# Kernel optimization log

Measured on AMD Instinct MI355X. Metric: run time of the kernel, lower is better.

The kernel has to match this reference:

```python
import jax, jax.numpy as jnp
import numpy as np

B, N, D, M = 16, 4096, 640, 64  # D = hidden_dim*2 + u_in = 2*256 + 128


def setup_inputs() -> dict:
    key = jax.random.key(0)
    kx, kk, kv = jax.random.split(key, 3)
    x = jax.random.normal(kx, (B, N, D), dtype=jnp.float32)
    Mk = jax.random.normal(kk, (M, D), dtype=jnp.float32)
    Mv = jax.random.normal(kv, (M, D), dtype=jnp.float32)
    return {"x": x, "Mk": Mk, "Mv": Mv}


def reference(x, Mk, Mv):
    # scores: [B, N, M] = x @ Mk^T
    scores = jnp.einsum('bnd,md->bnm', x, Mk)
    weights = jax.nn.softmax(scores, axis=-1)
    # out: [B, N, D] = weights @ Mv
    out = jnp.einsum('bnm,md->bnd', weights, Mv)
    return out
```

## Files before the change

kernel.cpp:

```cpp
#include <hip/hip_runtime.h>

typedef float  f32x4  __attribute__((ext_vector_type(4)));
typedef short  short8 __attribute__((ext_vector_type(8)));
typedef __bf16 bf16x8 __attribute__((ext_vector_type(8)));

#define DEV static __device__ __forceinline__

DEV f32x4 mfma16(short8 a, short8 b, f32x4 c) {
  return __builtin_amdgcn_mfma_f32_16x16x32_bf16(
      __builtin_bit_cast(bf16x8, a), __builtin_bit_cast(bf16x8, b), c, 0, 0, 0);
}

DEV void splitf(float f, unsigned short& hi, unsigned short& lo) {
  unsigned u = __builtin_bit_cast(unsigned, f);
  hi = (unsigned short)(u >> 16);
  float hf = __builtin_bit_cast(float, u & 0xFFFF0000u);
  float r = f - hf;
  unsigned v = __builtin_bit_cast(unsigned, r);
  lo = (unsigned short)((v + 0x7FFFu + ((v >> 16) & 1u)) >> 16);
}

#define DDIM 640
#define KCH  20
#define MKP_ELEMS (KCH*2*4*64*8)
#define MVP_OFF   MKP_ELEMS

__global__ void ea_pack(const float* __restrict__ Mk, const float* __restrict__ Mv,
                        unsigned short* __restrict__ ws) {
  int tid = blockIdx.x * 256 + threadIdx.x;
  unsigned short* MkP = ws;
  unsigned short* MvP = ws + MVP_OFF;
  if (tid < 5120) {
    int c = tid >> 8;
    int g = (tid >> 6) & 3;
    int l = tid & 63;
    int t = l & 15, q = l >> 4;
    const float* src = Mk + (16*g + t) * DDIM + 32*c + 8*q;
    unsigned short* dh = MkP + (((c*2 + 0)*4 + g)*64 + l)*8;
    unsigned short* dl = MkP + (((c*2 + 1)*4 + g)*64 + l)*8;
#pragma unroll
    for (int j = 0; j < 8; ++j) splitf(src[j], dh[j], dl[j]);
  } else if (tid < 10240) {
    int s = tid - 5120;
    int n = s >> 7;
    int c = (s >> 6) & 1;
    int l = s & 63;
    int t = l & 15, q = l >> 4;
    const float* src = Mv + (32*c + 8*q) * DDIM + 16*n + t;
    unsigned short* dh = MvP + (((n*2 + c)*2 + 0)*64 + l)*8;
    unsigned short* dl = MvP + (((n*2 + c)*2 + 1)*64 + l)*8;
#pragma unroll
    for (int j = 0; j < 8; ++j) splitf(src[j*DDIM], dh[j], dl[j]);
  }
}

#define LOADX(X0, X1, c) { X0 = *(const f32x4*)(xp + 32*(c)); \
                           X1 = *(const f32x4*)(xp + 32*(c) + 4); }

#define LOADF(c) { const unsigned short* mkc_ = MkP + (c)*4096 + l*8;        \
  fh0 = *(const short8*)(mkc_);        fh1 = *(const short8*)(mkc_ + 512);   \
  fh2 = *(const short8*)(mkc_ + 1024); fh3 = *(const short8*)(mkc_ + 1536);  \
  fl0 = *(const short8*)(mkc_ + 2048); fl1 = *(const short8*)(mkc_ + 2560);  \
  fl2 = *(const short8*)(mkc_ + 3072); fl3 = *(const short8*)(mkc_ + 3584); }

#define SPLITX(X0, X1)                                                       \
  splitf(X0[0], ah.u[0], al.u[0]); splitf(X0[1], ah.u[1], al.u[1]);          \
  splitf(X0[2], ah.u[2], al.u[2]); splitf(X0[3], ah.u[3], al.u[3]);          \
  splitf(X1[0], ah.u[4], al.u[4]); splitf(X1[1], ah.u[5], al.u[5]);          \
  splitf(X1[2], ah.u[6], al.u[6]); splitf(X1[3], ah.u[7], al.u[7]);

#define MFMAS()                                                              \
  acc[0] = mfma16(ah.s, fh0, acc[0]); acc[1] = mfma16(ah.s, fh1, acc[1]);    \
  acc[2] = mfma16(ah.s, fh2, acc[2]); acc[3] = mfma16(ah.s, fh3, acc[3]);    \
  acc[0] = mfma16(al.s, fh0, acc[0]); acc[1] = mfma16(al.s, fh1, acc[1]);    \
  acc[2] = mfma16(al.s, fh2, acc[2]); acc[3] = mfma16(al.s, fh3, acc[3]);    \
  acc[0] = mfma16(ah.s, fl0, acc[0]); acc[1] = mfma16(ah.s, fl1, acc[1]);    \
  acc[2] = mfma16(ah.s, fl2, acc[2]); acc[3] = mfma16(ah.s, fl3, acc[3]);

__global__ __launch_bounds__(64, 4) void ea_main(const float* __restrict__ x,
                                                 const unsigned short* __restrict__ MkP,
                                                 const unsigned short* __restrict__ MvP,
                                                 float* __restrict__ out) {
  __shared__ __align__(16) unsigned short Wh[16][64];
  __shared__ __align__(16) unsigned short Wl[16][64];
  const int l = threadIdx.x;
  const int t = l & 15;
  const int q = l >> 4;
  const long row0 = (long)blockIdx.x * 16;

  const float* xp = x + (row0 + t) * DDIM + 8*q;
  f32x4 acc[4];
#pragma unroll
  for (int g = 0; g < 4; ++g) acc[g] = (f32x4){0.f, 0.f, 0.f, 0.f};

  f32x4 x00,x01,x10,x11,x20,x21,x30,x31;
  short8 fh0,fh1,fh2,fh3, fl0,fl1,fl2,fl3;
  union { short8 s; unsigned short u[8]; } ah, al;

  LOADX(x00,x01, 0) LOADX(x10,x11, 1) LOADX(x20,x21, 2) LOADX(x30,x31, 3)

#pragma unroll
  for (int cc = 0; cc < KCH; cc += 4) {
    const bool pf = (cc + 4 < KCH);
    LOADF(cc)     SPLITX(x00, x01) if (pf) { LOADX(x00,x01, cc+4) } MFMAS()
    LOADF(cc+1)   SPLITX(x10, x11) if (pf) { LOADX(x10,x11, cc+5) } MFMAS()
    LOADF(cc+2)   SPLITX(x20, x21) if (pf) { LOADX(x20,x21, cc+6) } MFMAS()
    LOADF(cc+3)   SPLITX(x30, x31) if (pf) { LOADX(x30,x31, cc+7) } MFMAS()
  }

  float rmax[4], rsum[4];
#pragma unroll
  for (int j = 0; j < 4; ++j)
    rmax[j] = fmaxf(fmaxf(acc[0][j], acc[1][j]), fmaxf(acc[2][j], acc[3][j]));
#pragma unroll
  for (int mk = 1; mk <= 8; mk <<= 1) {
#pragma unroll
    for (int j = 0; j < 4; ++j)
      rmax[j] = fmaxf(rmax[j], __shfl_xor(rmax[j], mk, 64));
  }
#pragma unroll
  for (int g = 0; g < 4; ++g)
#pragma unroll
    for (int j = 0; j < 4; ++j)
      acc[g][j] = exp2f((acc[g][j] - rmax[j]) * 1.44269504f);
#pragma unroll
  for (int j = 0; j < 4; ++j)
    rsum[j] = (acc[0][j] + acc[1][j]) + (acc[2][j] + acc[3][j]);
#pragma unroll
  for (int mk = 1; mk <= 8; mk <<= 1) {
#pragma unroll
    for (int j = 0; j < 4; ++j)
      rsum[j] += __shfl_xor(rsum[j], mk, 64);
  }
#pragma unroll
  for (int j = 0; j < 4; ++j) rsum[j] = 1.0f / rsum[j];

#pragma unroll
  for (int g = 0; g < 4; ++g)
#pragma unroll
    for (int j = 0; j < 4; ++j) {
      float wt = acc[g][j] * rsum[j];
      unsigned short hi, lo;
      splitf(wt, hi, lo);
      int row = 4*q + j;
      int ms  = (16*g + t) ^ ((row & 7) << 3);
      Wh[row][ms] = hi;
      Wl[row][ms] = lo;
    }
  asm volatile("s_waitcnt lgkmcnt(0)" ::: "memory");
  __builtin_amdgcn_sched_barrier(0);

  short8 aH0, aH1, aL0, aL1;
  {
    const int sw  = (t & 7) << 3;
    const int ms0 = (8*q) ^ sw;
    const int ms1 = (32 + 8*q) ^ sw;
    aH0 = *(const short8*)&Wh[t][ms0];
    aH1 = *(const short8*)&Wh[t][ms1];
    aL0 = *(const short8*)&Wl[t][ms0];
    aL1 = *(const short8*)&Wl[t][ms1];
  }

  short8 vAh0, vAh1, vAl0, vAl1, vBh0, vBh1, vBl0, vBl1;
  {
    const unsigned short* mvp = MvP + l*8;
    vAh0 = *(const short8*)(mvp);        vAl0 = *(const short8*)(mvp + 512);
    vAh1 = *(const short8*)(mvp + 1024); vAl1 = *(const short8*)(mvp + 1536);
  }
  float* opb = out + (row0 + 4*q) * DDIM + t;

#pragma unroll 2
  for (int n = 0; n < 40; n += 2) {
    {
      const unsigned short* mvp = MvP + (n + 1) * 2048 + l*8;
      vBh0 = *(const short8*)(mvp);        vBl0 = *(const short8*)(mvp + 512);
      vBh1 = *(const short8*)(mvp + 1024); vBl1 = *(const short8*)(mvp + 1536);
    }
    {
      f32x4 o = (f32x4){0.f,0.f,0.f,0.f};
      o = mfma16(aH0, vAh0, o); o = mfma16(aL0, vAh0, o); o = mfma16(aH0, vAl0, o);
      o = mfma16(aH1, vAh1, o); o = mfma16(aL1, vAh1, o); o = mfma16(aH1, vAl1, o);
      float* op = opb + 16*n;
#pragma unroll
      for (int j = 0; j < 4; ++j) __builtin_nontemporal_store(o[j], op + j*DDIM);
    }
    if (n + 2 < 40) {
      const unsigned short* mvp = MvP + (n + 2) * 2048 + l*8;
      vAh0 = *(const short8*)(mvp);        vAl0 = *(const short8*)(mvp + 512);
      vAh1 = *(const short8*)(mvp + 1024); vAl1 = *(const short8*)(mvp + 1536);
    }
    {
      f32x4 o = (f32x4){0.f,0.f,0.f,0.f};
      o = mfma16(aH0, vBh0, o); o = mfma16(aL0, vBh0, o); o = mfma16(aH0, vBl0, o);
      o = mfma16(aH1, vBh1, o); o = mfma16(aL1, vBh1, o); o = mfma16(aH1, vBl1, o);
      float* op = opb + 16*(n + 1);
#pragma unroll
      for (int j = 0; j < 4; ++j) __builtin_nontemporal_store(o[j], op + j*DDIM);
    }
  }
}

extern "C" void kernel_launch(void* const* d_in, const int* in_sizes, int n_in,
                              void* d_out, int out_size, void* d_ws, size_t ws_size,
                              hipStream_t stream) {
  const float* x  = (const float*)d_in[0];
  const float* Mk = (const float*)d_in[1];
  const float* Mv = (const float*)d_in[2];
  float* outp = (float*)d_out;
  unsigned short* ws = (unsigned short*)d_ws;

  ea_pack<<<40, 256, 0, stream>>>(Mk, Mv, ws);
  ea_main<<<4096, 64, 0, stream>>>(x, ws, ws + MVP_OFF, outp);
}
```

Baseline: 88.47 us.

## Share packed Mk/Mv tiles across four waves via double-buffered LDS staging

The kernel moves from one-wave blocks to four-wave blocks covering 64 rows. Each wave fetches a quarter of every packed Mk and Mv chunk into LDS with global_load_lds, double-buffered and separated by barriers. Before, every wave read the full Mk and Mv from global or L2 on its own, so this cuts that redundant traffic by sharing through LDS. The cost is per-chunk workgroup barriers that can stall waves, fewer blocks in flight, and output stores that are now ordinary rather than nontemporal.

```diff
diff --git a/kernel.cpp b/kernel.cpp
--- a/kernel.cpp
+++ b/kernel.cpp
@@ -5,6 +5,7 @@
 typedef __bf16 bf16x8 __attribute__((ext_vector_type(8)));
 
 #define DEV static __device__ __forceinline__
+#define SB  __builtin_amdgcn_sched_barrier(0)
 
 DEV f32x4 mfma16(short8 a, short8 b, f32x4 c) {
   return __builtin_amdgcn_mfma_f32_16x16x32_bf16(
@@ -18,6 +19,12 @@
   float r = f - hf;
   unsigned v = __builtin_bit_cast(unsigned, r);
   lo = (unsigned short)((v + 0x7FFFu + ((v >> 16) & 1u)) >> 16);
+}
+
+DEV void gload16(const unsigned short* g, unsigned short* lds) {
+  __builtin_amdgcn_global_load_lds(
+      (const __attribute__((address_space(1))) void*)g,
+      (__attribute__((address_space(3))) void*)lds, 16, 0, 0);
 }
 
 #define DDIM 640
@@ -57,12 +64,6 @@
 #define LOADX(X0, X1, c) { X0 = *(const f32x4*)(xp + 32*(c)); \
                            X1 = *(const f32x4*)(xp + 32*(c) + 4); }
 
-#define LOADF(c) { const unsigned short* mkc_ = MkP + (c)*4096 + l*8;        \
-  fh0 = *(const short8*)(mkc_);        fh1 = *(const short8*)(mkc_ + 512);   \
-  fh2 = *(const short8*)(mkc_ + 1024); fh3 = *(const short8*)(mkc_ + 1536);  \
-  fl0 = *(const short8*)(mkc_ + 2048); fl1 = *(const short8*)(mkc_ + 2560);  \
-  fl2 = *(const short8*)(mkc_ + 3072); fl3 = *(const short8*)(mkc_ + 3584); }
-
 #define SPLITX(X0, X1)                                                       \
   splitf(X0[0], ah.u[0], al.u[0]); splitf(X0[1], ah.u[1], al.u[1]);          \
   splitf(X0[2], ah.u[2], al.u[2]); splitf(X0[3], ah.u[3], al.u[3]);          \
@@ -77,16 +78,79 @@
   acc[0] = mfma16(ah.s, fl0, acc[0]); acc[1] = mfma16(ah.s, fl1, acc[1]);    \
   acc[2] = mfma16(ah.s, fl2, acc[2]); acc[3] = mfma16(ah.s, fl3, acc[3]);
 
-__global__ __launch_bounds__(64, 4) void ea_main(const float* __restrict__ x,
-                                                 const unsigned short* __restrict__ MkP,
-                                                 const unsigned short* __restrict__ MvP,
-                                                 float* __restrict__ out) {
-  __shared__ __align__(16) unsigned short Wh[16][64];
-  __shared__ __align__(16) unsigned short Wl[16][64];
-  const int l = threadIdx.x;
+#define G1_ITER(c, XA, XB) {                                                 \
+  SB;                                                                        \
+  if ((c) + 1 < KCH) {                                                       \
+    const unsigned short* gs = MkP + ((c)+1)*4096 + sgl;                     \
+    unsigned short* ld = &Stg[((c)+1) & 1][sgw];                             \
+    gload16(gs, ld); gload16(gs + 512, ld + 512);                            \
+  }                                                                          \
+  SB;                                                                        \
+  { const unsigned short* s_ = &Stg[(c) & 1][l*8];                           \
+    fh0 = *(const short8*)(s_);        fh1 = *(const short8*)(s_ + 512);     \
+    fh2 = *(const short8*)(s_ + 1024); fh3 = *(const short8*)(s_ + 1536);    \
+    fl0 = *(const short8*)(s_ + 2048); fl1 = *(const short8*)(s_ + 2560);    \
+    fl2 = *(const short8*)(s_ + 3072); fl3 = *(const short8*)(s_ + 3584);    \
+    SPLITX(XA, XB)                                                           \
+    SB;                                                                      \
+    if ((c) + 4 < KCH) { LOADX(XA, XB, (c)+4) }                              \
+    SB;                                                                      \
+    MFMAS() }                                                                \
+  SB;                                                                        \
+  asm volatile("s_waitcnt vmcnt(2)" ::: "memory");                           \
+  SB;                                                                        \
+  __builtin_amdgcn_s_barrier();                                              \
+  SB;                                                                        \
+}
+
+#define G2_PHASE(P, B) {                                                     \
+  SB;                                                                        \
+  if ((P) + 1 < 20) {                                                        \
+    const unsigned short* gs = MvP + ((P)+1)*4096 + sgl;                     \
+    unsigned short* ld = &Stg[(B) ^ 1][sgw];                                 \
+    gload16(gs, ld); gload16(gs + 512, ld + 512);                            \
+  }                                                                          \
+  SB;                                                                        \
+  { const unsigned short* s_ = &Stg[B][l*8];                                 \
+    short8 vh0 = *(const short8*)(s_);        short8 vl0 = *(const short8*)(s_ + 512);  \
+    short8 vh1 = *(const short8*)(s_ + 1024); short8 vl1 = *(const short8*)(s_ + 1536); \
+    short8 wh0 = *(const short8*)(s_ + 2048); short8 wl0 = *(const short8*)(s_ + 2560); \
+    short8 wh1 = *(const short8*)(s_ + 3072); short8 wl1 = *(const short8*)(s_ + 3584); \
+    f32x4 o0 = (f32x4){0.f,0.f,0.f,0.f};                                     \
+    o0 = mfma16(aH0, vh0, o0); o0 = mfma16(aL0, vh0, o0);                    \
+    o0 = mfma16(aH0, vl0, o0); o0 = mfma16(aH1, vh1, o0);                    \
+    o0 = mfma16(aL1, vh1, o0); o0 = mfma16(aH1, vl1, o0);                    \
+    f32x4 o1 = (f32x4){0.f,0.f,0.f,0.f};                                     \
+    o1 = mfma16(aH0, wh0, o1); o1 = mfma16(aL0, wh0, o1);                    \
+    o1 = mfma16(aH0, wl0, o1); o1 = mfma16(aH1, wh1, o1);                    \
+    o1 = mfma16(aL1, wh1, o1); o1 = mfma16(aH1, wl1, o1);                    \
+    float* p0 = opb + 32*(P);                                                \
+    float* p1 = p0 + 16;                                                     \
+    p0[0] = o0[0]; p0[DDIM] = o0[1]; p0[2*DDIM] = o0[2]; p0[3*DDIM] = o0[3]; \
+    p1[0] = o1[0]; p1[DDIM] = o1[1]; p1[2*DDIM] = o1[2]; p1[3*DDIM] = o1[3]; \
+  }                                                                          \
+  SB;                                                                        \
+  asm volatile("s_waitcnt vmcnt(8)" ::: "memory");                           \
+  SB;                                                                        \
+  __builtin_amdgcn_s_barrier();                                              \
+  SB;                                                                        \
+}
+
+__global__ __launch_bounds__(256, 4) void ea_main(const float* __restrict__ x,
+                                                  const unsigned short* __restrict__ MkP,
+                                                  const unsigned short* __restrict__ MvP,
+                                                  float* __restrict__ out) {
+  __shared__ __align__(16) unsigned short Stg[2][4096];
+  __shared__ __align__(16) unsigned short Wh[4][16][64];
+  __shared__ __align__(16) unsigned short Wl[4][16][64];
+  const int tid = threadIdx.x;
+  const int w = tid >> 6;
+  const int l = tid & 63;
   const int t = l & 15;
   const int q = l >> 4;
-  const long row0 = (long)blockIdx.x * 16;
+  const int sgl = w*1024 + l*8;
+  const int sgw = w*1024;
+  const long row0 = (long)blockIdx.x * 64 + 16*w;
 
   const float* xp = x + (row0 + t) * DDIM + 8*q;
   f32x4 acc[4];
@@ -97,16 +161,25 @@
   short8 fh0,fh1,fh2,fh3, fl0,fl1,fl2,fl3;
   union { short8 s; unsigned short u[8]; } ah, al;
 
+  SB;
+  gload16(MkP + sgl, &Stg[0][sgw]); gload16(MkP + sgl + 512, &Stg[0][sgw + 512]);
+  SB;
   LOADX(x00,x01, 0) LOADX(x10,x11, 1) LOADX(x20,x21, 2) LOADX(x30,x31, 3)
-
-#pragma unroll
-  for (int cc = 0; cc < KCH; cc += 4) {
-    const bool pf = (cc + 4 < KCH);
-    LOADF(cc)     SPLITX(x00, x01) if (pf) { LOADX(x00,x01, cc+4) } MFMAS()
-    LOADF(cc+1)   SPLITX(x10, x11) if (pf) { LOADX(x10,x11, cc+5) } MFMAS()
-    LOADF(cc+2)   SPLITX(x20, x21) if (pf) { LOADX(x20,x21, cc+6) } MFMAS()
-    LOADF(cc+3)   SPLITX(x30, x31) if (pf) { LOADX(x30,x31, cc+7) } MFMAS()
-  }
+  SB;
+  asm volatile("s_waitcnt vmcnt(8)" ::: "memory");
+  SB;
+  __builtin_amdgcn_s_barrier();
+  SB;
+
+  G1_ITER( 0,x00,x01) G1_ITER( 1,x10,x11) G1_ITER( 2,x20,x21) G1_ITER( 3,x30,x31)
+  G1_ITER( 4,x00,x01) G1_ITER( 5,x10,x11) G1_ITER( 6,x20,x21) G1_ITER( 7,x30,x31)
+  G1_ITER( 8,x00,x01) G1_ITER( 9,x10,x11) G1_ITER(10,x20,x21) G1_ITER(11,x30,x31)
+  G1_ITER(12,x00,x01) G1_ITER(13,x10,x11) G1_ITER(14,x20,x21) G1_ITER(15,x30,x31)
+  G1_ITER(16,x00,x01) G1_ITER(17,x10,x11) G1_ITER(18,x20,x21) G1_ITER(19,x30,x31)
+
+  SB;
+  gload16(MvP + sgl, &Stg[0][sgw]); gload16(MvP + sgl + 512, &Stg[0][sgw + 512]);
+  SB;
 
   float rmax[4], rsum[4];
 #pragma unroll
@@ -144,59 +217,33 @@
       splitf(wt, hi, lo);
       int row = 4*q + j;
       int ms  = (16*g + t) ^ ((row & 7) << 3);
-      Wh[row][ms] = hi;
-      Wl[row][ms] = lo;
+      Wh[w][row][ms] = hi;
+      Wl[w][row][ms] = lo;
     }
   asm volatile("s_waitcnt lgkmcnt(0)" ::: "memory");
-  __builtin_amdgcn_sched_barrier(0);
+  SB;
 
   short8 aH0, aH1, aL0, aL1;
   {
     const int sw  = (t & 7) << 3;
     const int ms0 = (8*q) ^ sw;
     const int ms1 = (32 + 8*q) ^ sw;
-    aH0 = *(const short8*)&Wh[t][ms0];
-    aH1 = *(const short8*)&Wh[t][ms1];
-    aL0 = *(const short8*)&Wl[t][ms0];
-    aL1 = *(const short8*)&Wl[t][ms1];
-  }
-
-  short8 vAh0, vAh1, vAl0, vAl1, vBh0, vBh1, vBl0, vBl1;
-  {
-    const unsigned short* mvp = MvP + l*8;
-    vAh0 = *(const short8*)(mvp);        vAl0 = *(const short8*)(mvp + 512);
-    vAh1 = *(const short8*)(mvp + 1024); vAl1 = *(const short8*)(mvp + 1536);
-  }
+    aH0 = *(const short8*)&Wh[w][t][ms0];
+    aH1 = *(const short8*)&Wh[w][t][ms1];
+    aL0 = *(const short8*)&Wl[w][t][ms0];
+    aL1 = *(const short8*)&Wl[w][t][ms1];
+  }
+  SB;
+  asm volatile("s_waitcnt vmcnt(0)" ::: "memory");
+  SB;
+  __builtin_amdgcn_s_barrier();
+  SB;
+
   float* opb = out + (row0 + 4*q) * DDIM + t;
-
-#pragma unroll 2
-  for (int n = 0; n < 40; n += 2) {
-    {
-      const unsigned short* mvp = MvP + (n + 1) * 2048 + l*8;
-      vBh0 = *(const short8*)(mvp);        vBl0 = *(const short8*)(mvp + 512);
-      vBh1 = *(const short8*)(mvp + 1024); vBl1 = *(const short8*)(mvp + 1536);
-    }
-    {
-      f32x4 o = (f32x4){0.f,0.f,0.f,0.f};
-      o = mfma16(aH0, vAh0, o); o = mfma16(aL0, vAh0, o); o = mfma16(aH0, vAl0, o);
-      o = mfma16(aH1, vAh1, o); o = mfma16(aL1, vAh1, o); o = mfma16(aH1, vAl1, o);
-      float* op = opb + 16*n;
-#pragma unroll
-      for (int j = 0; j < 4; ++j) __builtin_nontemporal_store(o[j], op + j*DDIM);
-    }
-    if (n + 2 < 40) {
-      const unsigned short* mvp = MvP + (n + 2) * 2048 + l*8;
-      vAh0 = *(const short8*)(mvp);        vAl0 = *(const short8*)(mvp + 512);
-      vAh1 = *(const short8*)(mvp + 1024); vAl1 = *(const short8*)(mvp + 1536);
-    }
-    {
-      f32x4 o = (f32x4){0.f,0.f,0.f,0.f};
-      o = mfma16(aH0, vBh0, o); o = mfma16(aL0, vBh0, o); o = mfma16(aH0, vBl0, o);
-      o = mfma16(aH1, vBh1, o); o = mfma16(aL1, vBh1, o); o = mfma16(aH1, vBl1, o);
-      float* op = opb + 16*(n + 1);
-#pragma unroll
-      for (int j = 0; j < 4; ++j) __builtin_nontemporal_store(o[j], op + j*DDIM);
-    }
+#pragma unroll 1
+  for (int pp = 0; pp < 20; pp += 2) {
+    G2_PHASE(pp,     0)
+    G2_PHASE(pp + 1, 1)
   }
 }
 
@@ -210,5 +257,5 @@
   unsigned short* ws = (unsigned short*)d_ws;
 
   ea_pack<<<40, 256, 0, stream>>>(Mk, Mv, ws);
-  ea_main<<<4096, 64, 0, stream>>>(x, ws, ws + MVP_OFF, outp);
-}
+  ea_main<<<1024, 256, 0, stream>>>(x, ws, ws + MVP_OFF, outp);
+}
```

Result: slower. 94.49 us (+6.8%).

## Split D across two wavefronts per block with LDS partial-score reduction

Applied to the files above, without the earlier changes.

Each 16-row block now runs two wavefronts. Each wave computes partial scores over half of the 640 columns, and the partials are summed through shared memory. The softmax is then done cooperatively, with each lane handling 8 columns of one row and writing packed bf16 hi/lo weights. Each wave then produces half of the output columns. This doubles the parallelism per row tile and halves each wave's serial chain, at the cost of extra LDS traffic and two block barriers. It also adds sched_barriers around the first-GEMM stages and replaces nontemporal output stores with plain stores.

```diff
diff --git a/kernel.cpp b/kernel.cpp
--- a/kernel.cpp
+++ b/kernel.cpp
@@ -5,6 +5,7 @@
 typedef __bf16 bf16x8 __attribute__((ext_vector_type(8)));
 
 #define DEV static __device__ __forceinline__
+#define SB  __builtin_amdgcn_sched_barrier(0)
 
 DEV f32x4 mfma16(short8 a, short8 b, f32x4 c) {
   return __builtin_amdgcn_mfma_f32_16x16x32_bf16(
@@ -54,14 +55,8 @@
   }
 }
 
-#define LOADX(X0, X1, c) { X0 = *(const f32x4*)(xp + 32*(c)); \
-                           X1 = *(const f32x4*)(xp + 32*(c) + 4); }
-
-#define LOADF(c) { const unsigned short* mkc_ = MkP + (c)*4096 + l*8;        \
-  fh0 = *(const short8*)(mkc_);        fh1 = *(const short8*)(mkc_ + 512);   \
-  fh2 = *(const short8*)(mkc_ + 1024); fh3 = *(const short8*)(mkc_ + 1536);  \
-  fl0 = *(const short8*)(mkc_ + 2048); fl1 = *(const short8*)(mkc_ + 2560);  \
-  fl2 = *(const short8*)(mkc_ + 3072); fl3 = *(const short8*)(mkc_ + 3584); }
+#define LOADX(X0, X1, i) { X0 = *(const f32x4*)(xp + 32*(i)); \
+                           X1 = *(const f32x4*)(xp + 32*(i) + 4); }
 
 #define SPLITX(X0, X1)                                                       \
   splitf(X0[0], ah.u[0], al.u[0]); splitf(X0[1], ah.u[1], al.u[1]);          \
@@ -77,78 +72,88 @@
   acc[0] = mfma16(ah.s, fl0, acc[0]); acc[1] = mfma16(ah.s, fl1, acc[1]);    \
   acc[2] = mfma16(ah.s, fl2, acc[2]); acc[3] = mfma16(ah.s, fl3, acc[3]);
 
-__global__ __launch_bounds__(64, 4) void ea_main(const float* __restrict__ x,
-                                                 const unsigned short* __restrict__ MkP,
-                                                 const unsigned short* __restrict__ MvP,
-                                                 float* __restrict__ out) {
+#define G1_IT(i, X0, X1) {                                                   \
+  SB;                                                                        \
+  { const unsigned short* s_ = mkb + (i)*4096 + l*8;                         \
+    fh0 = *(const short8*)(s_);        fh1 = *(const short8*)(s_ + 512);     \
+    fh2 = *(const short8*)(s_ + 1024); fh3 = *(const short8*)(s_ + 1536);    \
+    fl0 = *(const short8*)(s_ + 2048); fl1 = *(const short8*)(s_ + 2560);    \
+    fl2 = *(const short8*)(s_ + 3072); fl3 = *(const short8*)(s_ + 3584);    \
+    SB;                                                                      \
+    SPLITX(X0, X1)                                                           \
+    SB;                                                                      \
+    if ((i) + 2 < 10) { LOADX(X0, X1, (i)+2) }                               \
+    SB;                                                                      \
+    MFMAS() }                                                                \
+  SB;                                                                        \
+}
+
+__global__ __launch_bounds__(128, 6) void ea_main(const float* __restrict__ x,
+                                                  const unsigned short* __restrict__ MkP,
+                                                  const unsigned short* __restrict__ MvP,
+                                                  float* __restrict__ out) {
+  __shared__ float Pld[2][16][68];
   __shared__ __align__(16) unsigned short Wh[16][64];
   __shared__ __align__(16) unsigned short Wl[16][64];
-  const int l = threadIdx.x;
+  const int tid = threadIdx.x;
+  const int h = tid >> 6;
+  const int l = tid & 63;
   const int t = l & 15;
   const int q = l >> 4;
   const long row0 = (long)blockIdx.x * 16;
 
-  const float* xp = x + (row0 + t) * DDIM + 8*q;
+  const float* xp = x + (row0 + t) * DDIM + 320*h + 8*q;
+  const unsigned short* mkb = MkP + (10*h) * 4096;
   f32x4 acc[4];
 #pragma unroll
   for (int g = 0; g < 4; ++g) acc[g] = (f32x4){0.f, 0.f, 0.f, 0.f};
 
-  f32x4 x00,x01,x10,x11,x20,x21,x30,x31;
+  f32x4 xA0, xA1, xB0, xB1;
   short8 fh0,fh1,fh2,fh3, fl0,fl1,fl2,fl3;
   union { short8 s; unsigned short u[8]; } ah, al;
 
-  LOADX(x00,x01, 0) LOADX(x10,x11, 1) LOADX(x20,x21, 2) LOADX(x30,x31, 3)
-
-#pragma unroll
-  for (int cc = 0; cc < KCH; cc += 4) {
-    const bool pf = (cc + 4 < KCH);
-    LOADF(cc)     SPLITX(x00, x01) if (pf) { LOADX(x00,x01, cc+4) } MFMAS()
-    LOADF(cc+1)   SPLITX(x10, x11) if (pf) { LOADX(x10,x11, cc+5) } MFMAS()
-    LOADF(cc+2)   SPLITX(x20, x21) if (pf) { LOADX(x20,x21, cc+6) } MFMAS()
-    LOADF(cc+3)   SPLITX(x30, x31) if (pf) { LOADX(x30,x31, cc+7) } MFMAS()
-  }
-
-  float rmax[4], rsum[4];
-#pragma unroll
-  for (int j = 0; j < 4; ++j)
-    rmax[j] = fmaxf(fmaxf(acc[0][j], acc[1][j]), fmaxf(acc[2][j], acc[3][j]));
-#pragma unroll
-  for (int mk = 1; mk <= 8; mk <<= 1) {
+  LOADX(xA0,xA1, 0) LOADX(xB0,xB1, 1)
+  G1_IT(0, xA0,xA1) G1_IT(1, xB0,xB1)
+  G1_IT(2, xA0,xA1) G1_IT(3, xB0,xB1)
+  G1_IT(4, xA0,xA1) G1_IT(5, xB0,xB1)
+  G1_IT(6, xA0,xA1) G1_IT(7, xB0,xB1)
+  G1_IT(8, xA0,xA1) G1_IT(9, xB0,xB1)
+
+#pragma unroll
+  for (int g = 0; g < 4; ++g)
 #pragma unroll
     for (int j = 0; j < 4; ++j)
-      rmax[j] = fmaxf(rmax[j], __shfl_xor(rmax[j], mk, 64));
-  }
-#pragma unroll
-  for (int g = 0; g < 4; ++g)
-#pragma unroll
-    for (int j = 0; j < 4; ++j)
-      acc[g][j] = exp2f((acc[g][j] - rmax[j]) * 1.44269504f);
-#pragma unroll
-  for (int j = 0; j < 4; ++j)
-    rsum[j] = (acc[0][j] + acc[1][j]) + (acc[2][j] + acc[3][j]);
-#pragma unroll
-  for (int mk = 1; mk <= 8; mk <<= 1) {
-#pragma unroll
-    for (int j = 0; j < 4; ++j)
-      rsum[j] += __shfl_xor(rsum[j], mk, 64);
-  }
-#pragma unroll
-  for (int j = 0; j < 4; ++j) rsum[j] = 1.0f / rsum[j];
-
-#pragma unroll
-  for (int g = 0; g < 4; ++g)
-#pragma unroll
-    for (int j = 0; j < 4; ++j) {
-      float wt = acc[g][j] * rsum[j];
-      unsigned short hi, lo;
-      splitf(wt, hi, lo);
-      int row = 4*q + j;
-      int ms  = (16*g + t) ^ ((row & 7) << 3);
-      Wh[row][ms] = hi;
-      Wl[row][ms] = lo;
-    }
-  asm volatile("s_waitcnt lgkmcnt(0)" ::: "memory");
-  __builtin_amdgcn_sched_barrier(0);
+      Pld[h][4*q + j][16*g + t] = acc[g][j];
+  __syncthreads();
+
+  {
+    const int R = 8*h + (l >> 3);
+    const int s = l & 7;
+    f32x4 a0 = *(const f32x4*)&Pld[0][R][8*s];
+    f32x4 a1 = *(const f32x4*)&Pld[0][R][8*s + 4];
+    f32x4 b0 = *(const f32x4*)&Pld[1][R][8*s];
+    f32x4 b1 = *(const f32x4*)&Pld[1][R][8*s + 4];
+    f32x4 v0 = a0 + b0, v1 = a1 + b1;
+    float mx = fmaxf(fmaxf(fmaxf(v0[0], v0[1]), fmaxf(v0[2], v0[3])),
+                     fmaxf(fmaxf(v1[0], v1[1]), fmaxf(v1[2], v1[3])));
+#pragma unroll
+    for (int mk = 1; mk <= 4; mk <<= 1) mx = fmaxf(mx, __shfl_xor(mx, mk, 64));
+    float pv[8], sum = 0.f;
+#pragma unroll
+    for (int j = 0; j < 4; ++j) { pv[j]   = exp2f((v0[j] - mx) * 1.44269504f); sum += pv[j]; }
+#pragma unroll
+    for (int j = 0; j < 4; ++j) { pv[4+j] = exp2f((v1[j] - mx) * 1.44269504f); sum += pv[4+j]; }
+#pragma unroll
+    for (int mk = 1; mk <= 4; mk <<= 1) sum += __shfl_xor(sum, mk, 64);
+    float inv = 1.0f / sum;
+    union { short8 s8; unsigned short u[8]; } wh, wl;
+#pragma unroll
+    for (int j = 0; j < 8; ++j) splitf(pv[j] * inv, wh.u[j], wl.u[j]);
+    const int gr = (s ^ (R & 7)) * 8;
+    *(short8*)&Wh[R][gr] = wh.s8;
+    *(short8*)&Wl[R][gr] = wl.s8;
+  }
+  __syncthreads();
 
   short8 aH0, aH1, aL0, aL1;
   {
@@ -161,18 +166,19 @@
     aL1 = *(const short8*)&Wl[t][ms1];
   }
 
+  const unsigned short* mvb = MvP + (20*h) * 2048;
   short8 vAh0, vAh1, vAl0, vAl1, vBh0, vBh1, vBl0, vBl1;
   {
-    const unsigned short* mvp = MvP + l*8;
+    const unsigned short* mvp = mvb + l*8;
     vAh0 = *(const short8*)(mvp);        vAl0 = *(const short8*)(mvp + 512);
     vAh1 = *(const short8*)(mvp + 1024); vAl1 = *(const short8*)(mvp + 1536);
   }
-  float* opb = out + (row0 + 4*q) * DDIM + t;
+  float* opb = out + (row0 + 4*q) * DDIM + 320*h + t;
 
 #pragma unroll 2
-  for (int n = 0; n < 40; n += 2) {
+  for (int n = 0; n < 20; n += 2) {
     {
-      const unsigned short* mvp = MvP + (n + 1) * 2048 + l*8;
+      const unsigned short* mvp = mvb + (n + 1) * 2048 + l*8;
       vBh0 = *(const short8*)(mvp);        vBl0 = *(const short8*)(mvp + 512);
       vBh1 = *(const short8*)(mvp + 1024); vBl1 = *(const short8*)(mvp + 1536);
     }
@@ -182,10 +188,10 @@
       o = mfma16(aH1, vAh1, o); o = mfma16(aL1, vAh1, o); o = mfma16(aH1, vAl1, o);
       float* op = opb + 16*n;
 #pragma unroll
-      for (int j = 0; j < 4; ++j) __builtin_nontemporal_store(o[j], op + j*DDIM);
-    }
-    if (n + 2 < 40) {
-      const unsigned short* mvp = MvP + (n + 2) * 2048 + l*8;
+      for (int j = 0; j < 4; ++j) op[j * DDIM] = o[j];
+    }
+    if (n + 2 < 20) {
+      const unsigned short* mvp = mvb + (n + 2) * 2048 + l*8;
       vAh0 = *(const short8*)(mvp);        vAl0 = *(const short8*)(mvp + 512);
       vAh1 = *(const short8*)(mvp + 1024); vAl1 = *(const short8*)(mvp + 1536);
     }
@@ -195,7 +201,7 @@
       o = mfma16(aH1, vBh1, o); o = mfma16(aL1, vBh1, o); o = mfma16(aH1, vBl1, o);
       float* op = opb + 16*(n + 1);
 #pragma unroll
-      for (int j = 0; j < 4; ++j) __builtin_nontemporal_store(o[j], op + j*DDIM);
+      for (int j = 0; j < 4; ++j) op[j * DDIM] = o[j];
     }
   }
 }
@@ -210,5 +216,5 @@
   unsigned short* ws = (unsigned short*)d_ws;
 
   ea_pack<<<40, 256, 0, stream>>>(Mk, Mv, ws);
-  ea_main<<<4096, 64, 0, stream>>>(x, ws, ws + MVP_OFF, outp);
-}
+  ea_main<<<4096, 128, 0, stream>>>(x, ws, ws + MVP_OFF, outp);
+}
```

Result: slower. 183.8 us (+107.7%).

## Double-buffer Mk fragments with sched barriers and transpose output MFMA for vector stores

Applied to the files above, without the earlier changes.

The first GEMM stage now uses two register sets of Mk fragments, loading chunk c+1 while chunk c is multiplied, with a three-deep x prefetch and explicit sched_barriers pinning the order. The second GEMM swaps its MFMA operands so each lane holds four consecutive output columns. Scalar nontemporal stores become 16-byte vector stores. This costs more registers for the extra fragment set and drops the nontemporal hint on output writes.

```diff
diff --git a/kernel.cpp b/kernel.cpp
--- a/kernel.cpp
+++ b/kernel.cpp
@@ -5,6 +5,7 @@
 typedef __bf16 bf16x8 __attribute__((ext_vector_type(8)));
 
 #define DEV static __device__ __forceinline__
+#define SB  __builtin_amdgcn_sched_barrier(0)
 
 DEV f32x4 mfma16(short8 a, short8 b, f32x4 c) {
   return __builtin_amdgcn_mfma_f32_16x16x32_bf16(
@@ -57,11 +58,17 @@
 #define LOADX(X0, X1, c) { X0 = *(const f32x4*)(xp + 32*(c)); \
                            X1 = *(const f32x4*)(xp + 32*(c) + 4); }
 
-#define LOADF(c) { const unsigned short* mkc_ = MkP + (c)*4096 + l*8;        \
-  fh0 = *(const short8*)(mkc_);        fh1 = *(const short8*)(mkc_ + 512);   \
-  fh2 = *(const short8*)(mkc_ + 1024); fh3 = *(const short8*)(mkc_ + 1536);  \
-  fl0 = *(const short8*)(mkc_ + 2048); fl1 = *(const short8*)(mkc_ + 2560);  \
-  fl2 = *(const short8*)(mkc_ + 3072); fl3 = *(const short8*)(mkc_ + 3584); }
+#define LOADFA(c) { const unsigned short* p_ = MkP + (c)*4096 + l8;          \
+  fa0 = *(const short8*)(p_);        fa1 = *(const short8*)(p_ + 512);       \
+  fa2 = *(const short8*)(p_ + 1024); fa3 = *(const short8*)(p_ + 1536);      \
+  fa4 = *(const short8*)(p_ + 2048); fa5 = *(const short8*)(p_ + 2560);     \
+  fa6 = *(const short8*)(p_ + 3072); fa7 = *(const short8*)(p_ + 3584); }
+
+#define LOADFB(c) { const unsigned short* p_ = MkP + (c)*4096 + l8;          \
+  fb0 = *(const short8*)(p_);        fb1 = *(const short8*)(p_ + 512);       \
+  fb2 = *(const short8*)(p_ + 1024); fb3 = *(const short8*)(p_ + 1536);      \
+  fb4 = *(const short8*)(p_ + 2048); fb5 = *(const short8*)(p_ + 2560);     \
+  fb6 = *(const short8*)(p_ + 3072); fb7 = *(const short8*)(p_ + 3584); }
 
 #define SPLITX(X0, X1)                                                       \
   splitf(X0[0], ah.u[0], al.u[0]); splitf(X0[1], ah.u[1], al.u[1]);          \
@@ -69,13 +76,33 @@
   splitf(X1[0], ah.u[4], al.u[4]); splitf(X1[1], ah.u[5], al.u[5]);          \
   splitf(X1[2], ah.u[6], al.u[6]); splitf(X1[3], ah.u[7], al.u[7]);
 
-#define MFMAS()                                                              \
-  acc[0] = mfma16(ah.s, fh0, acc[0]); acc[1] = mfma16(ah.s, fh1, acc[1]);    \
-  acc[2] = mfma16(ah.s, fh2, acc[2]); acc[3] = mfma16(ah.s, fh3, acc[3]);    \
-  acc[0] = mfma16(al.s, fh0, acc[0]); acc[1] = mfma16(al.s, fh1, acc[1]);    \
-  acc[2] = mfma16(al.s, fh2, acc[2]); acc[3] = mfma16(al.s, fh3, acc[3]);    \
-  acc[0] = mfma16(ah.s, fl0, acc[0]); acc[1] = mfma16(ah.s, fl1, acc[1]);    \
-  acc[2] = mfma16(ah.s, fl2, acc[2]); acc[3] = mfma16(ah.s, fl3, acc[3]);
+#define MFMAS_A()                                                            \
+  acc[0] = mfma16(ah.s, fa0, acc[0]); acc[1] = mfma16(ah.s, fa1, acc[1]);    \
+  acc[2] = mfma16(ah.s, fa2, acc[2]); acc[3] = mfma16(ah.s, fa3, acc[3]);    \
+  acc[0] = mfma16(al.s, fa0, acc[0]); acc[1] = mfma16(al.s, fa1, acc[1]);    \
+  acc[2] = mfma16(al.s, fa2, acc[2]); acc[3] = mfma16(al.s, fa3, acc[3]);    \
+  acc[0] = mfma16(ah.s, fa4, acc[0]); acc[1] = mfma16(ah.s, fa5, acc[1]);    \
+  acc[2] = mfma16(ah.s, fa6, acc[2]); acc[3] = mfma16(ah.s, fa7, acc[3]);
+
+#define MFMAS_B()                                                            \
+  acc[0] = mfma16(ah.s, fb0, acc[0]); acc[1] = mfma16(ah.s, fb1, acc[1]);    \
+  acc[2] = mfma16(ah.s, fb2, acc[2]); acc[3] = mfma16(ah.s, fb3, acc[3]);    \
+  acc[0] = mfma16(al.s, fb0, acc[0]); acc[1] = mfma16(al.s, fb1, acc[1]);    \
+  acc[2] = mfma16(al.s, fb2, acc[2]); acc[3] = mfma16(al.s, fb3, acc[3]);    \
+  acc[0] = mfma16(ah.s, fb4, acc[0]); acc[1] = mfma16(ah.s, fb5, acc[1]);    \
+  acc[2] = mfma16(ah.s, fb6, acc[2]); acc[3] = mfma16(ah.s, fb7, acc[3]);
+
+#define G1A(c, X0, X1, PF, PX) {                                             \
+  SB; if (PF) { LOADFB((c)+1) } SB;                                          \
+  SPLITX(X0, X1) SB;                                                         \
+  if (PX) { LOADX(X0, X1, (c)+3) } SB;                                       \
+  MFMAS_A() SB; }
+
+#define G1B(c, X0, X1, PF, PX) {                                             \
+  SB; if (PF) { LOADFA((c)+1) } SB;                                          \
+  SPLITX(X0, X1) SB;                                                         \
+  if (PX) { LOADX(X0, X1, (c)+3) } SB;                                       \
+  MFMAS_B() SB; }
 
 __global__ __launch_bounds__(64, 4) void ea_main(const float* __restrict__ x,
                                                  const unsigned short* __restrict__ MkP,
@@ -86,6 +113,7 @@
   const int l = threadIdx.x;
   const int t = l & 15;
   const int q = l >> 4;
+  const int l8 = l * 8;
   const long row0 = (long)blockIdx.x * 16;
 
   const float* xp = x + (row0 + t) * DDIM + 8*q;
@@ -93,20 +121,23 @@
 #pragma unroll
   for (int g = 0; g < 4; ++g) acc[g] = (f32x4){0.f, 0.f, 0.f, 0.f};
 
-  f32x4 x00,x01,x10,x11,x20,x21,x30,x31;
-  short8 fh0,fh1,fh2,fh3, fl0,fl1,fl2,fl3;
+  f32x4 x00,x01,x10,x11,x20,x21;
+  short8 fa0,fa1,fa2,fa3,fa4,fa5,fa6,fa7;
+  short8 fb0,fb1,fb2,fb3,fb4,fb5,fb6,fb7;
   union { short8 s; unsigned short u[8]; } ah, al;
 
-  LOADX(x00,x01, 0) LOADX(x10,x11, 1) LOADX(x20,x21, 2) LOADX(x30,x31, 3)
-
-#pragma unroll
-  for (int cc = 0; cc < KCH; cc += 4) {
-    const bool pf = (cc + 4 < KCH);
-    LOADF(cc)     SPLITX(x00, x01) if (pf) { LOADX(x00,x01, cc+4) } MFMAS()
-    LOADF(cc+1)   SPLITX(x10, x11) if (pf) { LOADX(x10,x11, cc+5) } MFMAS()
-    LOADF(cc+2)   SPLITX(x20, x21) if (pf) { LOADX(x20,x21, cc+6) } MFMAS()
-    LOADF(cc+3)   SPLITX(x30, x31) if (pf) { LOADX(x30,x31, cc+7) } MFMAS()
-  }
+  LOADX(x00,x01, 0) LOADX(x10,x11, 1) LOADX(x20,x21, 2)
+  SB;
+  LOADFA(0)
+  SB;
+
+  G1A( 0, x00,x01, 1, 1)  G1B( 1, x10,x11, 1, 1)  G1A( 2, x20,x21, 1, 1)
+  G1B( 3, x00,x01, 1, 1)  G1A( 4, x10,x11, 1, 1)  G1B( 5, x20,x21, 1, 1)
+  G1A( 6, x00,x01, 1, 1)  G1B( 7, x10,x11, 1, 1)  G1A( 8, x20,x21, 1, 1)
+  G1B( 9, x00,x01, 1, 1)  G1A(10, x10,x11, 1, 1)  G1B(11, x20,x21, 1, 1)
+  G1A(12, x00,x01, 1, 1)  G1B(13, x10,x11, 1, 1)  G1A(14, x20,x21, 1, 1)
+  G1B(15, x00,x01, 1, 1)  G1A(16, x10,x11, 1, 1)  G1B(17, x20,x21, 1, 0)
+  G1A(18, x00,x01, 1, 0)  G1B(19, x10,x11, 0, 0)
 
   float rmax[4], rsum[4];
 #pragma unroll
@@ -148,7 +179,7 @@
       Wl[row][ms] = lo;
     }
   asm volatile("s_waitcnt lgkmcnt(0)" ::: "memory");
-  __builtin_amdgcn_sched_barrier(0);
+  SB;
 
   short8 aH0, aH1, aL0, aL1;
   {
@@ -160,42 +191,39 @@
     aL0 = *(const short8*)&Wl[t][ms0];
     aL1 = *(const short8*)&Wl[t][ms1];
   }
+  SB;
 
   short8 vAh0, vAh1, vAl0, vAl1, vBh0, vBh1, vBl0, vBl1;
   {
-    const unsigned short* mvp = MvP + l*8;
+    const unsigned short* mvp = MvP + l8;
     vAh0 = *(const short8*)(mvp);        vAl0 = *(const short8*)(mvp + 512);
     vAh1 = *(const short8*)(mvp + 1024); vAl1 = *(const short8*)(mvp + 1536);
   }
-  float* opb = out + (row0 + 4*q) * DDIM + t;
+  float* opb = out + (row0 + t) * DDIM + 4*q;
 
 #pragma unroll 2
   for (int n = 0; n < 40; n += 2) {
     {
-      const unsigned short* mvp = MvP + (n + 1) * 2048 + l*8;
+      const unsigned short* mvp = MvP + (n + 1) * 2048 + l8;
       vBh0 = *(const short8*)(mvp);        vBl0 = *(const short8*)(mvp + 512);
       vBh1 = *(const short8*)(mvp + 1024); vBl1 = *(const short8*)(mvp + 1536);
     }
     {
       f32x4 o = (f32x4){0.f,0.f,0.f,0.f};
-      o = mfma16(aH0, vAh0, o); o = mfma16(aL0, vAh0, o); o = mfma16(aH0, vAl0, o);
-      o = mfma16(aH1, vAh1, o); o = mfma16(aL1, vAh1, o); o = mfma16(aH1, vAl1, o);
-      float* op = opb + 16*n;
-#pragma unroll
-      for (int j = 0; j < 4; ++j) __builtin_nontemporal_store(o[j], op + j*DDIM);
+      o = mfma16(vAh0, aH0, o); o = mfma16(vAh0, aL0, o); o = mfma16(vAl0, aH0, o);
+      o = mfma16(vAh1, aH1, o); o = mfma16(vAh1, aL1, o); o = mfma16(vAl1, aH1, o);
+      *(f32x4*)(opb + 16*n) = o;
     }
     if (n + 2 < 40) {
-      const unsigned short* mvp = MvP + (n + 2) * 2048 + l*8;
+      const unsigned short* mvp = MvP + (n + 2) * 2048 + l8;
       vAh0 = *(const short8*)(mvp);        vAl0 = *(const short8*)(mvp + 512);
       vAh1 = *(const short8*)(mvp + 1024); vAl1 = *(const short8*)(mvp + 1536);
     }
     {
       f32x4 o = (f32x4){0.f,0.f,0.f,0.f};
-      o = mfma16(aH0, vBh0, o); o = mfma16(aL0, vBh0, o); o = mfma16(aH0, vBl0, o);
-      o = mfma16(aH1, vBh1, o); o = mfma16(aL1, vBh1, o); o = mfma16(aH1, vBl1, o);
-      float* op = opb + 16*(n + 1);
-#pragma unroll
-      for (int j = 0; j < 4; ++j) __builtin_nontemporal_store(o[j], op + j*DDIM);
+      o = mfma16(vBh0, aH0, o); o = mfma16(vBh0, aL0, o); o = mfma16(vBl0, aH0, o);
+      o = mfma16(vBh1, aH1, o); o = mfma16(vBh1, aL1, o); o = mfma16(vBl1, aH1, o);
+      *(f32x4*)(opb + 16*(n + 1)) = o;
     }
   }
 }
```

Result: slower. 149.0 us (+68.4%).
